# Kernel tuning notes

Measured on AMD Instinct MI355X. Metric: run time of the kernel, lower is better.

Reference implementation:

```python
import jax, jax.numpy as jnp
import numpy as np
from jax import lax

B, T, D, L = 64, 512, 1024, 32


def setup_inputs() -> dict:
    key = jax.random.key(0)
    ks = jax.random.split(key, 6)
    embeddings = jax.random.normal(ks[0], (B, T, D), dtype=jnp.float32)
    W = jax.random.normal(ks[1], (L, D), dtype=jnp.float32) * (1.0 / np.sqrt(D))
    b = jnp.zeros((L,), dtype=jnp.float32)
    start_trans = jax.random.normal(ks[2], (L,), dtype=jnp.float32) * 0.1
    end_trans = jax.random.normal(ks[3], (L,), dtype=jnp.float32) * 0.1
    trans = jax.random.normal(ks[4], (L, L), dtype=jnp.float32) * 0.1
    labels = jax.random.randint(ks[5], (B, T), 0, L, dtype=jnp.int32)
    mask = jnp.ones((B, T), dtype=bool)  # torchcrf requires mask[:, 0] == True
    return {"embeddings": embeddings, "W": W, "b": b,
            "start_trans": start_trans, "end_trans": end_trans,
            "trans": trans, "labels": labels, "mask": mask}


def _crf_nll(emissions, labels, mask, start_trans, end_trans, trans):
    # emissions: [B, T, L]; torchcrf works time-first internally.
    em = jnp.transpose(emissions, (1, 0, 2))          # [T, B, L]
    tg = labels.T                                      # [T, B]
    mk_b = mask.T                                      # [T, B] bool
    mk_f = mk_b.astype(emissions.dtype)
    bidx = jnp.arange(em.shape[1])

    # ---- numerator: score of the gold tag path ----
    score0 = start_trans[tg[0]] + em[0, bidx, tg[0]]   # [B]

    def num_step(carry, inp):
        prev_tag, score = carry
        e_t, tag_t, m_b, m_f = inp
        step = trans[prev_tag, tag_t] + e_t[bidx, tag_t]
        score = score + step * m_f
        prev_tag = jnp.where(m_b, tag_t, prev_tag)
        return (prev_tag, score), None

    (last_tag, num), _ = lax.scan(num_step, (tg[0], score0),
                                  (em[1:], tg[1:], mk_b[1:], mk_f[1:]))
    num = num + end_trans[last_tag]

    # ---- denominator: forward algorithm (log partition) ----
    alpha0 = start_trans[None, :] + em[0]              # [B, L]

    def den_step(alpha, inp):
        e_t, m_b = inp
        # alpha[b, i] + trans[i, j] + e_t[b, j] -> logsumexp over i
        nxt = jax.nn.logsumexp(alpha[:, :, None] + trans[None, :, :]
                               + e_t[:, None, :], axis=1)
        alpha = jnp.where(m_b[:, None], nxt, alpha)
        return alpha, None

    alpha, _ = lax.scan(den_step, alpha0, (em[1:], mk_b[1:]))
    den = jax.nn.logsumexp(alpha + end_trans[None, :], axis=1)  # [B]

    llh = num - den                                    # log-likelihood per seq
    return -jnp.mean(llh)                              # reduction='mean', negated


def reference(embeddings, W, b, start_trans, end_trans, trans, labels, mask):
    # dropout is identity at eval time
    emissions = jnp.einsum('btd,ld->btl', embeddings, W) + b  # [B, T, L]
    return _crf_nll(emissions, labels, mask, start_trans, end_trans, trans)
```

## Files before the change

### kernel.cpp

```cpp
#include <hip/hip_runtime.h>
#include <hip/hip_bf16.h>

#define NB 64
#define NT 512
#define ND 1024
#define NL 32
#define SEG 16
#define NSEG 32

typedef __attribute__((ext_vector_type(8)))  short bf16x8;
typedef __attribute__((ext_vector_type(4)))  float f32x4;
typedef __attribute__((ext_vector_type(16))) float f32x16;

__device__ __forceinline__ unsigned short bfh(float x) {
    __hip_bfloat16 h = __float2bfloat16(x);
    return *(unsigned short*)&h;
}
__device__ __forceinline__ float frombf(unsigned short u) {
    return __uint_as_float(((unsigned)u) << 16);
}
__device__ __forceinline__ bf16x8 pack8(float4 x, float4 y) {
    bf16x8 r;
    unsigned short* p = (unsigned short*)&r;
    p[0] = bfh(x.x); p[1] = bfh(x.y); p[2] = bfh(x.z); p[3] = bfh(x.w);
    p[4] = bfh(y.x); p[5] = bfh(y.y); p[6] = bfh(y.z); p[7] = bfh(y.w);
    return r;
}

__global__ __launch_bounds__(256) void wb_kernel(
    const float* __restrict__ W, unsigned short* __restrict__ Wb)
{
    int i = blockIdx.x * 256 + threadIdx.x;
    float4 v = ((const float4*)W)[i];
    ushort4 o;
    o.x = bfh(v.x); o.y = bfh(v.y); o.z = bfh(v.z); o.w = bfh(v.w);
    ((ushort4*)Wb)[i] = o;
}

struct Grp {
    float4 a[4][2];
    bf16x8 b[4][2];
};

__device__ __forceinline__ void load_grp(
    Grp& G, const float* __restrict__ ap,
    const unsigned short* __restrict__ bp0,
    const unsigned short* __restrict__ bp1, int k0)
{
#pragma unroll
    for (int s = 0; s < 4; s++) {
        G.a[s][0] = *(const float4*)(ap + k0 + s * 32);
        G.a[s][1] = *(const float4*)(ap + k0 + s * 32 + 4);
        G.b[s][0] = *(const bf16x8*)(bp0 + k0 + s * 32);
        G.b[s][1] = *(const bf16x8*)(bp1 + k0 + s * 32);
    }
}

__global__ __launch_bounds__(256) void emseg_kernel(
    const float* __restrict__ emb,
    const unsigned short* __restrict__ Wb,
    const float* __restrict__ bias,
    const float* __restrict__ start_trans,
    const float* __restrict__ trans,
    const int*   __restrict__ labels,
    float* __restrict__ Pm,
    int*   __restrict__ exps,
    float* __restrict__ numpart)
{
    __shared__ float          em_s[4][SEG][36];
    __shared__ unsigned short Thi_s[4][32][40];
    __shared__ unsigned short Tlo_s[4][32][40];

    const int tid  = threadIdx.x;
    const int wv   = tid >> 6;
    const int lane = tid & 63;
    const int m    = lane & 15;
    const int quad = lane >> 4;
    const int w    = blockIdx.x * 4 + wv;
    const int b    = w >> 5;
    const int s    = w & 31;
    const int row  = w * 16 + m;
    const int t0   = s * SEG;

    const float*          ap  = emb + (size_t)row * ND + quad * 8;
    const unsigned short* bp0 = Wb + (size_t)m * ND + quad * 8;
    const unsigned short* bp1 = Wb + (size_t)(16 + m) * ND + quad * 8;

    f32x4 acc0 = {0.f, 0.f, 0.f, 0.f};
    f32x4 acc1 = {0.f, 0.f, 0.f, 0.f};

    Grp g0, g1;
    load_grp(g0, ap, bp0, bp1, 0);
    load_grp(g1, ap, bp0, bp1, 128);

#pragma unroll
    for (int g = 0; g < 8; g++) {
        Grp& cur = (g & 1) ? g1 : g0;
#pragma unroll
        for (int st = 0; st < 4; st++) {
            bf16x8 af = pack8(cur.a[st][0], cur.a[st][1]);
            acc0 = __builtin_amdgcn_mfma_f32_16x16x32_bf16(af, cur.b[st][0], acc0, 0, 0, 0);
            acc1 = __builtin_amdgcn_mfma_f32_16x16x32_bf16(af, cur.b[st][1], acc1, 0, 0, 0);
        }
        if (g < 6) load_grp(cur, ap, bp0, bp1, (g + 2) * 128);
    }

    const float bl0 = bias[m];
    const float bl1 = bias[16 + m];
#pragma unroll
    for (int r = 0; r < 4; r++) {
        int lt = quad * 4 + r;
        em_s[wv][lt][m]      = __expf(acc0[r] + bl0);
        em_s[wv][lt][16 + m] = __expf(acc1[r] + bl1);
    }
    asm volatile("s_waitcnt lgkmcnt(0)" ::: "memory");

    {
        const int* lab = labels + b * NT;
        float npart = 0.f;
        if (lane < SEG) {
            int t = t0 + lane;
            if (t >= 1) {
                int pt = lab[t - 1], ct = lab[t];
                npart = trans[pt * NL + ct] + __logf(em_s[wv][lane][ct]);
            } else {
                int c0 = lab[0];
                npart = start_trans[c0] + __logf(em_s[wv][0][c0]);
            }
        }
#pragma unroll
        for (int mk = 32; mk >= 1; mk >>= 1) npart += __shfl_xor(npart, mk, 64);
        if (lane == 0) numpart[b * NSEG + s] = npart;
    }

    const int col = lane & 31;
    const int h   = lane >> 5;
    const int ls  = (s == 0) ? 1 : 0;

    float Ecol[16];
#pragma unroll
    for (int j = 0; j < 8; j++) Ecol[j]     = __expf(trans[(8 * h + j) * NL + col]);
#pragma unroll
    for (int j = 0; j < 8; j++) Ecol[8 + j] = __expf(trans[(16 + 8 * h + j) * NL + col]);

    bf16x8 Ah1, Ah2, Al1, Al2;
    {
        float sA = 1.f;
        if (s == 0) sA = __expf(start_trans[col]) * em_s[wv][0][col];
#pragma unroll
        for (int j = 0; j < 8; j++) {
            int k1 = 8 * h + j, k2 = 16 + 8 * h + j;
            float v1 = sA * __expf(trans[col * NL + k1]) * em_s[wv][ls][k1];
            float v2 = sA * __expf(trans[col * NL + k2]) * em_s[wv][ls][k2];
            unsigned short h1 = bfh(v1), h2 = bfh(v2);
            ((unsigned short*)&Ah1)[j] = h1;
            ((unsigned short*)&Ah2)[j] = h2;
            ((unsigned short*)&Al1)[j] = bfh(v1 - frombf(h1));
            ((unsigned short*)&Al2)[j] = bfh(v2 - frombf(h2));
        }
    }

    int eseg = 0;
    for (int lt = ls + 1; lt < SEG; lt++) {
        float emn = em_s[wv][lt][col];
        bf16x8 Bh1, Bh2, Bl1, Bl2;
#pragma unroll
        for (int j = 0; j < 8; j++) {
            float v1 = Ecol[j] * emn;
            float v2 = Ecol[8 + j] * emn;
            unsigned short h1 = bfh(v1), h2 = bfh(v2);
            ((unsigned short*)&Bh1)[j] = h1;
            ((unsigned short*)&Bh2)[j] = h2;
            ((unsigned short*)&Bl1)[j] = bfh(v1 - frombf(h1));
            ((unsigned short*)&Bl2)[j] = bfh(v2 - frombf(h2));
        }

        f32x16 acc;
#pragma unroll
        for (int i = 0; i < 16; i++) acc[i] = 0.f;
        acc = __builtin_amdgcn_mfma_f32_32x32x16_bf16(Ah1, Bh1, acc, 0, 0, 0);
        acc = __builtin_amdgcn_mfma_f32_32x32x16_bf16(Ah2, Bh2, acc, 0, 0, 0);
        acc = __builtin_amdgcn_mfma_f32_32x32x16_bf16(Ah1, Bl1, acc, 0, 0, 0);
        acc = __builtin_amdgcn_mfma_f32_32x32x16_bf16(Ah2, Bl2, acc, 0, 0, 0);
        acc = __builtin_amdgcn_mfma_f32_32x32x16_bf16(Al1, Bh1, acc, 0, 0, 0);
        acc = __builtin_amdgcn_mfma_f32_32x32x16_bf16(Al2, Bh2, acc, 0, 0, 0);

        int bits = __builtin_amdgcn_readlane(__float_as_int(acc[0]), 0);
        int e = (bits >> 23) & 255;
        eseg += e - 127;
        float scale = __uint_as_float((unsigned)(254 - e) << 23);

        if (lt < SEG - 1) {
#pragma unroll
            for (int r = 0; r < 16; r++) {
                int rowi = (r & 3) + 8 * (r >> 2) + 4 * h;
                float v = acc[r] * scale;
                unsigned short hi = bfh(v);
                Thi_s[wv][rowi][col] = hi;
                Tlo_s[wv][rowi][col] = bfh(v - frombf(hi));
            }
            asm volatile("s_waitcnt lgkmcnt(0)" ::: "memory");
            Ah1 = *(const bf16x8*)&Thi_s[wv][col][8 * h];
            Ah2 = *(const bf16x8*)&Thi_s[wv][col][16 + 8 * h];
            Al1 = *(const bf16x8*)&Tlo_s[wv][col][8 * h];
            Al2 = *(const bf16x8*)&Tlo_s[wv][col][16 + 8 * h];
        } else {
            float* dst = Pm + ((size_t)(b * NSEG + s) << 10);
#pragma unroll
            for (int r = 0; r < 16; r++) {
                int rowi = (r & 3) + 8 * (r >> 2) + 4 * h;
                dst[rowi * 32 + col] = acc[r] * scale;
            }
        }
    }
    if (lane == 0) exps[b * NSEG + s] = eseg;
}

__global__ __launch_bounds__(64) void comb_kernel(
    const float* __restrict__ end_trans,
    const float* __restrict__ Pm,
    const int*   __restrict__ exps,
    const float* __restrict__ numpart,
    const int*   __restrict__ labels,
    float* __restrict__ den_out,
    float* __restrict__ num_out)
{
    const int b    = blockIdx.x;
    const int lane = threadIdx.x;
    const int col  = lane & 31;

    int sexp = 0;
    float sv[32];
#pragma unroll
    for (int i = 0; i < 32; i++) sv[i] = 1.0f;

    const float* Pb = Pm + ((size_t)b * NSEG << 10);
    float Pc[32];
#pragma unroll
    for (int i = 0; i < 32; i++) Pc[i] = Pb[i * 32 + col];

    float a = 0.f;
    for (int s = 0; s < NSEG; s++) {
        float nb[32];
        if (s + 1 < NSEG) {
            const float* q = Pb + ((s + 1) << 10);
#pragma unroll
            for (int i = 0; i < 32; i++) nb[i] = q[i * 32 + col];
        } else {
#pragma unroll
            for (int i = 0; i < 32; i++) nb[i] = 0.f;
        }

        float p0 = sv[0] * Pc[0], p1 = sv[1] * Pc[1];
        float p2 = sv[2] * Pc[2], p3 = sv[3] * Pc[3];
        float p4 = sv[4] * Pc[4], p5 = sv[5] * Pc[5];
        float p6 = sv[6] * Pc[6], p7 = sv[7] * Pc[7];
#pragma unroll
        for (int i = 8; i < 32; i += 8) {
            p0 = fmaf(sv[i + 0], Pc[i + 0], p0);
            p1 = fmaf(sv[i + 1], Pc[i + 1], p1);
            p2 = fmaf(sv[i + 2], Pc[i + 2], p2);
            p3 = fmaf(sv[i + 3], Pc[i + 3], p3);
            p4 = fmaf(sv[i + 4], Pc[i + 4], p4);
            p5 = fmaf(sv[i + 5], Pc[i + 5], p5);
            p6 = fmaf(sv[i + 6], Pc[i + 6], p6);
            p7 = fmaf(sv[i + 7], Pc[i + 7], p7);
        }
        a = (((p0 + p1) + (p2 + p3)) + ((p4 + p5) + (p6 + p7)));

        int bits = __builtin_amdgcn_readlane(__float_as_int(a), 0);
        int e = (bits >> 23) & 255;
        sexp += e - 127;
        a *= __uint_as_float((unsigned)(254 - e) << 23);

#pragma unroll
        for (int i = 0; i < 32; i++)
            sv[i] = __int_as_float(__builtin_amdgcn_readlane(__float_as_int(a), i));
#pragma unroll
        for (int i = 0; i < 32; i++) Pc[i] = nb[i];
    }

    float sege = (lane < NSEG) ? (float)exps[b * NSEG + lane] : 0.f;
#pragma unroll
    for (int mk = 32; mk >= 1; mk >>= 1) sege += __shfl_xor(sege, mk, 64);

    float x = a * __expf(end_trans[col]);
#pragma unroll
    for (int mk = 16; mk >= 1; mk >>= 1) x += __shfl_xor(x, mk, 32);

    float nsum = (lane < NSEG) ? numpart[b * NSEG + lane] : 0.f;
#pragma unroll
    for (int mk = 32; mk >= 1; mk >>= 1) nsum += __shfl_xor(nsum, mk, 64);

    if (lane == 0) {
        int lT = labels[b * NT + NT - 1];
        num_out[b] = nsum + end_trans[lT];
        den_out[b] = __logf(x)
                   + 0.69314718055994531f * ((float)sexp + sege);
    }
}

__global__ __launch_bounds__(64) void fin_kernel(
    const float* __restrict__ den, const float* __restrict__ num,
    float* __restrict__ out)
{
    int lane = threadIdx.x;
    float v = den[lane] - num[lane];
#pragma unroll
    for (int mk = 32; mk >= 1; mk >>= 1) v += __shfl_xor(v, mk, 64);
    if (lane == 0) out[0] = v * (1.0f / 64.0f);
}

extern "C" void kernel_launch(void* const* d_in, const int* in_sizes, int n_in,
                              void* d_out, int out_size, void* d_ws, size_t ws_size,
                              hipStream_t stream)
{
    const float* emb    = (const float*)d_in[0];
    const float* W      = (const float*)d_in[1];
    const float* bias   = (const float*)d_in[2];
    const float* st     = (const float*)d_in[3];
    const float* en     = (const float*)d_in[4];
    const float* tr     = (const float*)d_in[5];
    const int*   labels = (const int*)d_in[6];

    char* p = (char*)d_ws;
    float* Pm  = (float*)p;                  p += (size_t)NB * NSEG * 1024 * 4;
    int*   exps = (int*)p;                   p += NB * NSEG * 4;
    float* nump = (float*)p;                 p += NB * NSEG * 4;
    float* den  = (float*)p;                 p += NB * 4;
    float* num  = (float*)p;                 p += NB * 4;
    unsigned short* Wb = (unsigned short*)p;
    float* out = (float*)d_out;

    wb_kernel   <<<(NL * ND) / 1024, 256, 0, stream>>>(W, Wb);
    emseg_kernel<<<(NB * NT) / 64, 256, 0, stream>>>(emb, Wb, bias, st, tr,
                                                     labels, Pm, exps, nump);
    comb_kernel <<<NB, 64, 0, stream>>>(en, Pm, exps, nump, labels, den, num);
    fin_kernel  <<<1, 64, 0, stream>>>(den, num, out);
}
```

Measured before the change: 236.1 us.

## Hoist emission scaling out of MFMA operand, split accumulators, fuse final reduction

```diff
diff --git a/kernel.cpp b/kernel.cpp
--- a/kernel.cpp
+++ b/kernel.cpp
@@ -28,8 +28,10 @@
 }
 
 __global__ __launch_bounds__(256) void wb_kernel(
-    const float* __restrict__ W, unsigned short* __restrict__ Wb)
-{
+    const float* __restrict__ W, unsigned short* __restrict__ Wb,
+    float* __restrict__ out)
+{
+    if (blockIdx.x == 0 && threadIdx.x == 0) out[0] = 0.f;
     int i = blockIdx.x * 256 + threadIdx.x;
     float4 v = ((const float4*)W)[i];
     ushort4 o;
@@ -137,21 +139,28 @@
     const int h   = lane >> 5;
     const int ls  = (s == 0) ? 1 : 0;
 
-    float Ecol[16];
-#pragma unroll
-    for (int j = 0; j < 8; j++) Ecol[j]     = __expf(trans[(8 * h + j) * NL + col]);
-#pragma unroll
-    for (int j = 0; j < 8; j++) Ecol[8 + j] = __expf(trans[(16 + 8 * h + j) * NL + col]);
+    bf16x8 Bh1, Bh2, Bl1, Bl2;
+#pragma unroll
+    for (int j = 0; j < 8; j++) {
+        float e1 = __expf(trans[(8 * h + j) * NL + col]);
+        float e2 = __expf(trans[(16 + 8 * h + j) * NL + col]);
+        unsigned short h1 = bfh(e1), h2 = bfh(e2);
+        ((unsigned short*)&Bh1)[j] = h1;
+        ((unsigned short*)&Bh2)[j] = h2;
+        ((unsigned short*)&Bl1)[j] = bfh(e1 - frombf(h1));
+        ((unsigned short*)&Bl2)[j] = bfh(e2 - frombf(h2));
+    }
 
     bf16x8 Ah1, Ah2, Al1, Al2;
     {
         float sA = 1.f;
         if (s == 0) sA = __expf(start_trans[col]) * em_s[wv][0][col];
+        const float* emt = em_s[wv][ls];
 #pragma unroll
         for (int j = 0; j < 8; j++) {
             int k1 = 8 * h + j, k2 = 16 + 8 * h + j;
-            float v1 = sA * __expf(trans[col * NL + k1]) * em_s[wv][ls][k1];
-            float v2 = sA * __expf(trans[col * NL + k2]) * em_s[wv][ls][k2];
+            float v1 = sA * __expf(trans[col * NL + k1]) * emt[k1];
+            float v2 = sA * __expf(trans[col * NL + k2]) * emt[k2];
             unsigned short h1 = bfh(v1), h2 = bfh(v2);
             ((unsigned short*)&Ah1)[j] = h1;
             ((unsigned short*)&Ah2)[j] = h2;
@@ -162,39 +171,28 @@
 
     int eseg = 0;
     for (int lt = ls + 1; lt < SEG; lt++) {
-        float emn = em_s[wv][lt][col];
-        bf16x8 Bh1, Bh2, Bl1, Bl2;
-#pragma unroll
-        for (int j = 0; j < 8; j++) {
-            float v1 = Ecol[j] * emn;
-            float v2 = Ecol[8 + j] * emn;
-            unsigned short h1 = bfh(v1), h2 = bfh(v2);
-            ((unsigned short*)&Bh1)[j] = h1;
-            ((unsigned short*)&Bh2)[j] = h2;
-            ((unsigned short*)&Bl1)[j] = bfh(v1 - frombf(h1));
-            ((unsigned short*)&Bl2)[j] = bfh(v2 - frombf(h2));
-        }
-
-        f32x16 acc;
-#pragma unroll
-        for (int i = 0; i < 16; i++) acc[i] = 0.f;
-        acc = __builtin_amdgcn_mfma_f32_32x32x16_bf16(Ah1, Bh1, acc, 0, 0, 0);
-        acc = __builtin_amdgcn_mfma_f32_32x32x16_bf16(Ah2, Bh2, acc, 0, 0, 0);
-        acc = __builtin_amdgcn_mfma_f32_32x32x16_bf16(Ah1, Bl1, acc, 0, 0, 0);
-        acc = __builtin_amdgcn_mfma_f32_32x32x16_bf16(Ah2, Bl2, acc, 0, 0, 0);
-        acc = __builtin_amdgcn_mfma_f32_32x32x16_bf16(Al1, Bh1, acc, 0, 0, 0);
-        acc = __builtin_amdgcn_mfma_f32_32x32x16_bf16(Al2, Bh2, acc, 0, 0, 0);
-
-        int bits = __builtin_amdgcn_readlane(__float_as_int(acc[0]), 0);
+        f32x16 aX, aY;
+#pragma unroll
+        for (int i = 0; i < 16; i++) { aX[i] = 0.f; aY[i] = 0.f; }
+        aX = __builtin_amdgcn_mfma_f32_32x32x16_bf16(Ah1, Bh1, aX, 0, 0, 0);
+        aY = __builtin_amdgcn_mfma_f32_32x32x16_bf16(Ah1, Bl1, aY, 0, 0, 0);
+        aX = __builtin_amdgcn_mfma_f32_32x32x16_bf16(Ah2, Bh2, aX, 0, 0, 0);
+        aY = __builtin_amdgcn_mfma_f32_32x32x16_bf16(Ah2, Bl2, aY, 0, 0, 0);
+        aX = __builtin_amdgcn_mfma_f32_32x32x16_bf16(Al1, Bh1, aX, 0, 0, 0);
+        aY = __builtin_amdgcn_mfma_f32_32x32x16_bf16(Al2, Bh2, aY, 0, 0, 0);
+
+        float c00 = aX[0] + aY[0];
+        int bits = __builtin_amdgcn_readlane(__float_as_int(c00), 0);
         int e = (bits >> 23) & 255;
         eseg += e - 127;
         float scale = __uint_as_float((unsigned)(254 - e) << 23);
+        float emsc = em_s[wv][lt][col] * scale;
 
         if (lt < SEG - 1) {
 #pragma unroll
             for (int r = 0; r < 16; r++) {
                 int rowi = (r & 3) + 8 * (r >> 2) + 4 * h;
-                float v = acc[r] * scale;
+                float v = (aX[r] + aY[r]) * emsc;
                 unsigned short hi = bfh(v);
                 Thi_s[wv][rowi][col] = hi;
                 Tlo_s[wv][rowi][col] = bfh(v - frombf(hi));
@@ -209,7 +207,7 @@
 #pragma unroll
             for (int r = 0; r < 16; r++) {
                 int rowi = (r & 3) + 8 * (r >> 2) + 4 * h;
-                dst[rowi * 32 + col] = acc[r] * scale;
+                dst[rowi * 32 + col] = (aX[r] + aY[r]) * emsc;
             }
         }
     }
@@ -222,8 +220,7 @@
     const int*   __restrict__ exps,
     const float* __restrict__ numpart,
     const int*   __restrict__ labels,
-    float* __restrict__ den_out,
-    float* __restrict__ num_out)
+    float* __restrict__ out)
 {
     const int b    = blockIdx.x;
     const int lane = threadIdx.x;
@@ -294,21 +291,10 @@
 
     if (lane == 0) {
         int lT = labels[b * NT + NT - 1];
-        num_out[b] = nsum + end_trans[lT];
-        den_out[b] = __logf(x)
-                   + 0.69314718055994531f * ((float)sexp + sege);
-    }
-}
-
-__global__ __launch_bounds__(64) void fin_kernel(
-    const float* __restrict__ den, const float* __restrict__ num,
-    float* __restrict__ out)
-{
-    int lane = threadIdx.x;
-    float v = den[lane] - num[lane];
-#pragma unroll
-    for (int mk = 32; mk >= 1; mk >>= 1) v += __shfl_xor(v, mk, 64);
-    if (lane == 0) out[0] = v * (1.0f / 64.0f);
+        float numv = nsum + end_trans[lT];
+        float denv = __logf(x) + 0.69314718055994531f * ((float)sexp + sege);
+        atomicAdd(out, (denv - numv) * (1.0f / 64.0f));
+    }
 }
 
 extern "C" void kernel_launch(void* const* d_in, const int* in_sizes, int n_in,
@@ -327,14 +313,11 @@
     float* Pm  = (float*)p;                  p += (size_t)NB * NSEG * 1024 * 4;
     int*   exps = (int*)p;                   p += NB * NSEG * 4;
     float* nump = (float*)p;                 p += NB * NSEG * 4;
-    float* den  = (float*)p;                 p += NB * 4;
-    float* num  = (float*)p;                 p += NB * 4;
     unsigned short* Wb = (unsigned short*)p;
     float* out = (float*)d_out;
 
-    wb_kernel   <<<(NL * ND) / 1024, 256, 0, stream>>>(W, Wb);
+    wb_kernel   <<<(NL * ND) / 1024, 256, 0, stream>>>(W, Wb, out);
     emseg_kernel<<<(NB * NT) / 64, 256, 0, stream>>>(emb, Wb, bias, st, tr,
                                                      labels, Pm, exps, nump);
-    comb_kernel <<<NB, 64, 0, stream>>>(en, Pm, exps, nump, labels, den, num);
-    fin_kernel  <<<1, 64, 0, stream>>>(den, num, out);
-}
+    comb_kernel <<<NB, 64, 0, stream>>>(en, Pm, exps, nump, labels, out);
+}
```

Result: no change. 237.3 us (+0.5%).
